# Kernel tuning notes

Hardware: AMD Instinct MI355X
Metric: run time of the kernel (lower is better)

Reference implementation:

```python
import jax, jax.numpy as jnp
import numpy as np

B, N, D = 8, 2048, 384

def setup_inputs() -> dict:
    key = jax.random.key(0)
    k1, k2, k3 = jax.random.split(key, 3)
    P_seq = jax.random.normal(k1, (B, N, D), dtype=jnp.float32)
    W = jax.random.normal(k2, (D, D), dtype=jnp.float32) / np.sqrt(D)
    b = jax.random.normal(k3, (1,), dtype=jnp.float32)
    return {"P_seq": P_seq, "W": W, "b": b}

def reference(P_seq, W, b):
    # nn.Bilinear(d, d, 1): logits[b,i,j] = P[b,i] @ W @ P[b,j] + bias
    # Efficient form: (P @ W) @ P^T, avoiding the O(B*N^2*D) expand.
    PW = jnp.einsum('bnd,de->bne', P_seq, W)          # [B, N, D]
    logits = jnp.einsum('bne,bme->bnm', PW, P_seq)    # [B, N, N]
    return logits + b[0]
```

## Files before the change

### kernel.cpp

```cpp
#include <hip/hip_runtime.h>
#include <stdint.h>


#define BATCH 8
#define NSEQ  2048
#define DDIM  384
#define BM 128
#define BN 128
#define BK 64

typedef __attribute__((ext_vector_type(8)))  _Float16 half8;
typedef __attribute__((ext_vector_type(4)))  _Float16 half4;
typedef __attribute__((ext_vector_type(16))) float    f32x16;

#define NP (BATCH * NSEQ * DDIM)
#define CAST_BLOCKS 1024

__global__ void prep_kernel(const float* __restrict__ P,
                            const float* __restrict__ W,
                            _Float16* __restrict__ Ph,
                            _Float16* __restrict__ Wt) {
    if (blockIdx.x < CAST_BLOCKS) {
        int i = (blockIdx.x * 256 + threadIdx.x) * 8;
        const int stride = CAST_BLOCKS * 256 * 8;
        for (; i < NP; i += stride) {
            float4 f0 = *(const float4*)(P + i);
            float4 f1 = *(const float4*)(P + i + 4);
            half8 h;
            h[0] = (_Float16)f0.x; h[1] = (_Float16)f0.y;
            h[2] = (_Float16)f0.z; h[3] = (_Float16)f0.w;
            h[4] = (_Float16)f1.x; h[5] = (_Float16)f1.y;
            h[6] = (_Float16)f1.z; h[7] = (_Float16)f1.w;
            *(half8*)(Ph + i) = h;
        }
    } else {
        int o = (blockIdx.x - CAST_BLOCKS) * 256 + threadIdx.x;
        if (o < DDIM * DDIM) {
            int e = o / DDIM;
            int d = o - e * DDIM;
            Wt[o] = (_Float16)W[d * DDIM + e];
        }
    }
}

__global__ __launch_bounds__(256, 4) void gemm1_kernel(
    const _Float16* __restrict__ A,
    const _Float16* __restrict__ Bmat,
    _Float16* __restrict__ C) {
    __shared__ _Float16 As[BM * BK];
    __shared__ _Float16 Bs[64 * BK];

    const int n   = blockIdx.x;
    const int xcd = n & 7;
    const int i2  = n >> 3;
    const int bx  = i2 % 6;
    const int by  = xcd + 8 * (i2 / 6);

    const _Float16* Ab = A + (size_t)by * BM * DDIM;
    const _Float16* Bb = Bmat + (size_t)bx * 64 * DDIM;

    const int tid  = threadIdx.x;
    const int wave = tid >> 6;
    const int lane = tid & 63;
    const int lm   = lane & 31;
    const int hi   = lane >> 5;

    const int srow = tid >> 3;
    const int scg  = ((tid & 7) ^ (srow & 7)) * 8;

    const int h0    = (hi ^ (lm & 7)) * 16;
    const int baseA = (wave * 32 + lm) * (BK * 2) + h0;
    const int baseB0 = lm * (BK * 2) + h0;
    const int baseB1 = (32 + lm) * (BK * 2) + h0;
    const char* AsB = (const char*)As;
    const char* BsB = (const char*)Bs;

    f32x16 acc0, acc1;
#pragma unroll
    for (int r = 0; r < 16; ++r) { acc0[r] = 0.f; acc1[r] = 0.f; }

    for (int k0 = 0; k0 < DDIM; k0 += BK) {
#pragma unroll
        for (int p = 0; p < 4; ++p) {
            __builtin_amdgcn_global_load_lds(
                (const __attribute__((address_space(1))) void*)
                    (Ab + (size_t)(p * 32 + srow) * DDIM + k0 + scg),
                (__attribute__((address_space(3))) void*)
                    (As + (p * 256 + tid) * 8),
                16, 0, 0);
        }
#pragma unroll
        for (int p = 0; p < 2; ++p) {
            __builtin_amdgcn_global_load_lds(
                (const __attribute__((address_space(1))) void*)
                    (Bb + (size_t)(p * 32 + srow) * DDIM + k0 + scg),
                (__attribute__((address_space(3))) void*)
                    (Bs + (p * 256 + tid) * 8),
                16, 0, 0);
        }
        __syncthreads();
#pragma unroll
        for (int s = 0; s < 4; ++s) {
            const int sx = s * 32;
            half8 a  = *(const half8*)(AsB + (baseA ^ sx));
            half8 b0 = *(const half8*)(BsB + (baseB0 ^ sx));
            half8 b1 = *(const half8*)(BsB + (baseB1 ^ sx));
            acc0 = __builtin_amdgcn_mfma_f32_32x32x16_f16(a, b0, acc0, 0, 0, 0);
            acc1 = __builtin_amdgcn_mfma_f32_32x32x16_f16(a, b1, acc1, 0, 0, 0);
        }
        __syncthreads();
    }

    const size_t row_base = (size_t)by * BM + wave * 32;
    const size_t col_base = (size_t)bx * 64;
#pragma unroll
    for (int reg = 0; reg < 16; ++reg) {
        const int rin = (reg & 3) + 8 * (reg >> 2) + 4 * hi;
        _Float16* row = C + (row_base + rin) * DDIM + col_base;
        row[lm]      = (_Float16)acc0[reg];
        row[32 + lm] = (_Float16)acc1[reg];
    }
}

__global__ __launch_bounds__(256, 4) void gemm2_kernel(
    const _Float16* __restrict__ A,
    const _Float16* __restrict__ Bmat,
    float* __restrict__ C,
    const float* __restrict__ bias_ptr) {
    __shared__ _Float16 As[BM * BK];
    __shared__ _Float16 Bs[BN * BK];

    const int n  = blockIdx.x;
    const int z  = n & 7;
    const int i2 = n >> 3;
    const int bx = i2 & 15;
    const int by = i2 >> 4;

    const size_t bstride = (size_t)NSEQ * DDIM;
    const _Float16* Ab = A + (size_t)z * bstride + (size_t)by * BM * DDIM;
    const _Float16* Bb = Bmat + (size_t)z * bstride + (size_t)bx * BN * DDIM;

    const int tid  = threadIdx.x;
    const int wave = tid >> 6;
    const int lane = tid & 63;
    const int wrow = wave >> 1;
    const int wcol = wave & 1;
    const int lm   = lane & 31;
    const int hi   = lane >> 5;

    const int srow = tid >> 3;
    const int scg  = ((tid & 7) ^ (srow & 7)) * 8;

    const int h0     = (hi ^ (lm & 7)) * 16;
    const int baseA0 = (wrow * 64 + lm) * (BK * 2) + h0;
    const int baseA1 = baseA0 + 32 * (BK * 2);
    const int baseB0 = (wcol * 64 + lm) * (BK * 2) + h0;
    const int baseB1 = baseB0 + 32 * (BK * 2);
    const char* AsB = (const char*)As;
    const char* BsB = (const char*)Bs;

    f32x16 acc[2][2];
#pragma unroll
    for (int i = 0; i < 2; ++i)
#pragma unroll
        for (int j = 0; j < 2; ++j)
#pragma unroll
            for (int r = 0; r < 16; ++r)
                acc[i][j][r] = 0.f;

    for (int k0 = 0; k0 < DDIM; k0 += BK) {
#pragma unroll
        for (int p = 0; p < 4; ++p) {
            const int r = p * 32 + srow;
            __builtin_amdgcn_global_load_lds(
                (const __attribute__((address_space(1))) void*)
                    (Ab + (size_t)r * DDIM + k0 + scg),
                (__attribute__((address_space(3))) void*)
                    (As + (p * 256 + tid) * 8),
                16, 0, 0);
            __builtin_amdgcn_global_load_lds(
                (const __attribute__((address_space(1))) void*)
                    (Bb + (size_t)r * DDIM + k0 + scg),
                (__attribute__((address_space(3))) void*)
                    (Bs + (p * 256 + tid) * 8),
                16, 0, 0);
        }
        __syncthreads();
#pragma unroll
        for (int s = 0; s < 4; ++s) {
            const int sx = s * 32;
            half8 a0 = *(const half8*)(AsB + (baseA0 ^ sx));
            half8 a1 = *(const half8*)(AsB + (baseA1 ^ sx));
            half8 b0 = *(const half8*)(BsB + (baseB0 ^ sx));
            half8 b1 = *(const half8*)(BsB + (baseB1 ^ sx));
            acc[0][0] = __builtin_amdgcn_mfma_f32_32x32x16_f16(a0, b0, acc[0][0], 0, 0, 0);
            acc[0][1] = __builtin_amdgcn_mfma_f32_32x32x16_f16(a0, b1, acc[0][1], 0, 0, 0);
            acc[1][0] = __builtin_amdgcn_mfma_f32_32x32x16_f16(a1, b0, acc[1][0], 0, 0, 0);
            acc[1][1] = __builtin_amdgcn_mfma_f32_32x32x16_f16(a1, b1, acc[1][1], 0, 0, 0);
        }
        __syncthreads();
    }

    const float bias = bias_ptr[0];
    float* Cb = C + (size_t)z * NSEQ * NSEQ;
    const size_t row_base = (size_t)by * BM + wrow * 64;
    const size_t col_base = (size_t)bx * BN + wcol * 64;
#pragma unroll
    for (int i = 0; i < 2; ++i)
#pragma unroll
        for (int j = 0; j < 2; ++j)
#pragma unroll
            for (int reg = 0; reg < 16; ++reg) {
                const int rin = (reg & 3) + 8 * (reg >> 2) + 4 * hi;
                Cb[(row_base + i * 32 + rin) * NSEQ
                   + col_base + j * 32 + lm] = acc[i][j][reg] + bias;
            }
}

extern "C" void kernel_launch(void* const* d_in, const int* in_sizes, int n_in,
                              void* d_out, int out_size, void* d_ws,
                              size_t ws_size, hipStream_t stream) {
    const float* P  = (const float*)d_in[0];
    const float* W  = (const float*)d_in[1];
    const float* bp = (const float*)d_in[2];
    float* out = (float*)d_out;

    _Float16* Ph = (_Float16*)d_ws;
    _Float16* Wt = Ph + (size_t)NP;
    _Float16* PW = Wt + (size_t)DDIM * DDIM;

    const int wblocks = (DDIM * DDIM + 255) / 256;
    prep_kernel<<<CAST_BLOCKS + wblocks, 256, 0, stream>>>(P, W, Ph, Wt);

    gemm1_kernel<<<768, 256, 0, stream>>>(Ph, Wt, PW);

    gemm2_kernel<<<2048, 256, 0, stream>>>(PW, Ph, out, bp);
}
```

Baseline: 185.0 us.

## Rewrite gemm2 with 256x256 tiles, double-buffered LDS and phased loads

The second GEMM now uses 256x256 output tiles with 512 threads (8 waves), each wave computing a 128x64 sub-tile. Operands go into double-buffered LDS, and global loads for the next K-slab are interleaved with MFMA phases using raw barriers, explicit vmcnt waits and s_setprio. Accumulators start at the bias value, which removes the epilogue add. The aim is more operand reuse per LDS byte and hiding global-load latency behind compute, at the cost of 128 KB of LDS per block, higher register pressure and only 512 blocks in the grid.

```diff
diff --git a/kernel.cpp b/kernel.cpp
--- a/kernel.cpp
+++ b/kernel.cpp
@@ -9,8 +9,10 @@
 #define BN 128
 #define BK 64
 
+#define G2_BM 256
+#define G2_BN 256
+
 typedef __attribute__((ext_vector_type(8)))  _Float16 half8;
-typedef __attribute__((ext_vector_type(4)))  _Float16 half4;
 typedef __attribute__((ext_vector_type(16))) float    f32x16;
 
 #define NP (BATCH * NSEQ * DDIM)
@@ -122,98 +124,158 @@
     }
 }
 
-__global__ __launch_bounds__(256, 4) void gemm2_kernel(
+
+#define G2_BAR() do { asm volatile("" ::: "memory");                       \
+    __builtin_amdgcn_s_barrier(); asm volatile("" ::: "memory"); } while (0)
+#define G2_VMW() asm volatile("s_waitcnt vmcnt(0)" ::: "memory")
+
+#define G2_STAGE_A(buf, k0)                                                \
+    _Pragma("unroll")                                                      \
+    for (int hl = 0; hl < 4; ++hl) {                                       \
+        __builtin_amdgcn_global_load_lds(                                  \
+            (const __attribute__((address_space(1))) void*)                \
+                (Ab + (size_t)(hl * 64 + srow) * DDIM + (k0) + scg),       \
+            (__attribute__((address_space(3))) void*)                      \
+                (&As[buf][0] + (hl * 512 + tid) * 8),                      \
+            16, 0, 0);                                                     \
+    }
+
+#define G2_STAGE_B(buf, k0)                                                \
+    _Pragma("unroll")                                                      \
+    for (int hl = 0; hl < 4; ++hl) {                                       \
+        __builtin_amdgcn_global_load_lds(                                  \
+            (const __attribute__((address_space(1))) void*)                \
+                (Bb + (size_t)(hl * 64 + srow) * DDIM + (k0) + scg),       \
+            (__attribute__((address_space(3))) void*)                      \
+                (&Bs[buf][0] + (hl * 512 + tid) * 8),                      \
+            16, 0, 0);                                                     \
+    }
+
+#define G2_PHASE(AP, BP, kh, mh, LOADB)                                    \
+    do {                                                                   \
+        if (LOADB) {                                                       \
+            _Pragma("unroll")                                              \
+            for (int nh = 0; nh < 2; ++nh)                                 \
+                _Pragma("unroll")                                          \
+                for (int k2 = 0; k2 < 2; ++k2)                             \
+                    bfrag[nh][k2] = *(const half8*)((BP)                   \
+                        + ((baseB + nh * 4096) ^ ((kh) * 64) ^ (k2 * 32)));\
+        }                                                                  \
+        half8 afr[2][2];                                                   \
+        _Pragma("unroll")                                                  \
+        for (int rs = 0; rs < 2; ++rs)                                     \
+            _Pragma("unroll")                                              \
+            for (int k2 = 0; k2 < 2; ++k2)                                 \
+                afr[rs][k2] = *(const half8*)((AP)                         \
+                    + ((baseA + (mh) * 8192 + rs * 4096)                   \
+                       ^ ((kh) * 64) ^ (k2 * 32)));                        \
+        __builtin_amdgcn_s_setprio(1);                                     \
+        _Pragma("unroll")                                                  \
+        for (int k2 = 0; k2 < 2; ++k2)                                     \
+            _Pragma("unroll")                                              \
+            for (int rs = 0; rs < 2; ++rs)                                 \
+                _Pragma("unroll")                                          \
+                for (int nh = 0; nh < 2; ++nh)                             \
+                    acc[(mh) * 2 + rs][nh] =                               \
+                        __builtin_amdgcn_mfma_f32_32x32x16_f16(            \
+                            afr[rs][k2], bfrag[nh][k2],                    \
+                            acc[(mh) * 2 + rs][nh], 0, 0, 0);              \
+        __builtin_amdgcn_s_setprio(0);                                     \
+    } while (0)
+
+__global__ __launch_bounds__(512, 2) void gemm2_kernel(
     const _Float16* __restrict__ A,
     const _Float16* __restrict__ Bmat,
     float* __restrict__ C,
     const float* __restrict__ bias_ptr) {
-    __shared__ _Float16 As[BM * BK];
-    __shared__ _Float16 Bs[BN * BK];
+    __shared__ _Float16 As[2][G2_BM * BK];
+    __shared__ _Float16 Bs[2][G2_BN * BK];
 
     const int n  = blockIdx.x;
     const int z  = n & 7;
     const int i2 = n >> 3;
-    const int bx = i2 & 15;
-    const int by = i2 >> 4;
+    const int bx = i2 & 7;
+    const int by = i2 >> 3;
 
     const size_t bstride = (size_t)NSEQ * DDIM;
-    const _Float16* Ab = A + (size_t)z * bstride + (size_t)by * BM * DDIM;
-    const _Float16* Bb = Bmat + (size_t)z * bstride + (size_t)bx * BN * DDIM;
+    const _Float16* Ab = A + (size_t)z * bstride + (size_t)by * G2_BM * DDIM;
+    const _Float16* Bb = Bmat + (size_t)z * bstride + (size_t)bx * G2_BN * DDIM;
 
     const int tid  = threadIdx.x;
     const int wave = tid >> 6;
     const int lane = tid & 63;
-    const int wrow = wave >> 1;
-    const int wcol = wave & 1;
+    const int wr   = wave >> 2;
+    const int wc   = wave & 3;
     const int lm   = lane & 31;
     const int hi   = lane >> 5;
 
     const int srow = tid >> 3;
     const int scg  = ((tid & 7) ^ (srow & 7)) * 8;
 
-    const int h0     = (hi ^ (lm & 7)) * 16;
-    const int baseA0 = (wrow * 64 + lm) * (BK * 2) + h0;
-    const int baseA1 = baseA0 + 32 * (BK * 2);
-    const int baseB0 = (wcol * 64 + lm) * (BK * 2) + h0;
-    const int baseB1 = baseB0 + 32 * (BK * 2);
-    const char* AsB = (const char*)As;
-    const char* BsB = (const char*)Bs;
-
-    f32x16 acc[2][2];
-#pragma unroll
-    for (int i = 0; i < 2; ++i)
-#pragma unroll
-        for (int j = 0; j < 2; ++j)
-#pragma unroll
-            for (int r = 0; r < 16; ++r)
-                acc[i][j][r] = 0.f;
-
-    for (int k0 = 0; k0 < DDIM; k0 += BK) {
-#pragma unroll
-        for (int p = 0; p < 4; ++p) {
-            const int r = p * 32 + srow;
-            __builtin_amdgcn_global_load_lds(
-                (const __attribute__((address_space(1))) void*)
-                    (Ab + (size_t)r * DDIM + k0 + scg),
-                (__attribute__((address_space(3))) void*)
-                    (As + (p * 256 + tid) * 8),
-                16, 0, 0);
-            __builtin_amdgcn_global_load_lds(
-                (const __attribute__((address_space(1))) void*)
-                    (Bb + (size_t)r * DDIM + k0 + scg),
-                (__attribute__((address_space(3))) void*)
-                    (Bs + (p * 256 + tid) * 8),
-                16, 0, 0);
-        }
-        __syncthreads();
-#pragma unroll
-        for (int s = 0; s < 4; ++s) {
-            const int sx = s * 32;
-            half8 a0 = *(const half8*)(AsB + (baseA0 ^ sx));
-            half8 a1 = *(const half8*)(AsB + (baseA1 ^ sx));
-            half8 b0 = *(const half8*)(BsB + (baseB0 ^ sx));
-            half8 b1 = *(const half8*)(BsB + (baseB1 ^ sx));
-            acc[0][0] = __builtin_amdgcn_mfma_f32_32x32x16_f16(a0, b0, acc[0][0], 0, 0, 0);
-            acc[0][1] = __builtin_amdgcn_mfma_f32_32x32x16_f16(a0, b1, acc[0][1], 0, 0, 0);
-            acc[1][0] = __builtin_amdgcn_mfma_f32_32x32x16_f16(a1, b0, acc[1][0], 0, 0, 0);
-            acc[1][1] = __builtin_amdgcn_mfma_f32_32x32x16_f16(a1, b1, acc[1][1], 0, 0, 0);
-        }
-        __syncthreads();
-    }
+    const int swz   = (hi ^ (lm & 7)) * 16;
+    const int baseA = (wr * 128 + lm) * (BK * 2) + swz;
+    const int baseB = (wc * 64 + lm) * (BK * 2) + swz;
+    const char* A0 = (const char*)&As[0][0];
+    const char* A1 = (const char*)&As[1][0];
+    const char* B0 = (const char*)&Bs[0][0];
+    const char* B1 = (const char*)&Bs[1][0];
 
     const float bias = bias_ptr[0];
+    f32x16 acc[4][2];
+#pragma unroll
+    for (int ri = 0; ri < 4; ++ri)
+#pragma unroll
+        for (int ci = 0; ci < 2; ++ci)
+#pragma unroll
+            for (int r = 0; r < 16; ++r) acc[ri][ci][r] = bias;
+
+    half8 bfrag[2][2];
+
+    G2_STAGE_A(0, 0);
+    G2_STAGE_B(0, 0);
+
+#pragma unroll
+    for (int it = 0; it < 3; ++it) {
+        const int kr1 = it * 128 + 64;
+        const int kn  = it * 128 + 128;
+
+        G2_VMW();
+        G2_BAR();
+        G2_STAGE_A(1, kr1);
+        G2_PHASE(A0, B0, 0, 0, 1);
+        G2_BAR();
+        G2_STAGE_B(1, kr1);
+        G2_PHASE(A0, B0, 0, 1, 0);
+        G2_BAR();
+        G2_PHASE(A0, B0, 1, 0, 1);
+        G2_BAR();
+        G2_PHASE(A0, B0, 1, 1, 0);
+
+        G2_VMW();
+        G2_BAR();
+        if (it < 2) G2_STAGE_A(0, kn);
+        G2_PHASE(A1, B1, 0, 0, 1);
+        G2_BAR();
+        if (it < 2) G2_STAGE_B(0, kn);
+        G2_PHASE(A1, B1, 0, 1, 0);
+        G2_BAR();
+        G2_PHASE(A1, B1, 1, 0, 1);
+        G2_BAR();
+        G2_PHASE(A1, B1, 1, 1, 0);
+    }
+
     float* Cb = C + (size_t)z * NSEQ * NSEQ;
-    const size_t row_base = (size_t)by * BM + wrow * 64;
-    const size_t col_base = (size_t)bx * BN + wcol * 64;
-#pragma unroll
-    for (int i = 0; i < 2; ++i)
-#pragma unroll
-        for (int j = 0; j < 2; ++j)
+    const size_t row_base = (size_t)by * G2_BM + wr * 128;
+    const size_t col_base = (size_t)bx * G2_BN + wc * 64;
+#pragma unroll
+    for (int ri = 0; ri < 4; ++ri)
+#pragma unroll
+        for (int ci = 0; ci < 2; ++ci)
 #pragma unroll
             for (int reg = 0; reg < 16; ++reg) {
                 const int rin = (reg & 3) + 8 * (reg >> 2) + 4 * hi;
-                Cb[(row_base + i * 32 + rin) * NSEQ
-                   + col_base + j * 32 + lm] = acc[i][j][reg] + bias;
+                Cb[(row_base + ri * 32 + rin) * NSEQ
+                   + col_base + ci * 32 + lm] = acc[ri][ci][reg];
             }
 }
 
@@ -234,5 +296,5 @@
 
     gemm1_kernel<<<768, 256, 0, stream>>>(Ph, Wt, PW);
 
-    gemm2_kernel<<<2048, 256, 0, stream>>>(PW, Ph, out, bp);
+    gemm2_kernel<<<512, 512, 0, stream>>>(PW, Ph, out, bp);
 }
```

After: 184.7 us. Within noise of the previous version (-0.1%).
